# Kernel tuning notes

Measured on AMD Instinct MI355X. Metric: run time of the kernel, lower is better.

The kernel has to match this reference:

```python
import jax, jax.numpy as jnp
import numpy as np

D = 2048      # hidden_size
W = 4         # kernel_size
DG = 2048     # generator hidden size (no reduction)

def setup_inputs() -> dict:
    key = jax.random.key(0)
    k1, k2, k3, k4 = jax.random.split(key, 4)
    x = jax.random.normal(k1, (2, 4096, D), dtype=jnp.float32)
    # Linear weights stored torch-style [out, in]; scaled small for sane activations
    w1 = jax.random.normal(k2, (DG, D), dtype=jnp.float32) * 0.02
    w2 = jax.random.normal(k3, (D * W, DG), dtype=jnp.float32) * 0.02
    b2 = jax.random.normal(k4, (D * W,), dtype=jnp.float32) * 0.02
    return {"x": x, "w1": w1, "w2": w2, "b2": b2}

def reference(x, w1, w2, b2):
    B, T, Dh = x.shape
    # kernel generator: w2(silu(w1 @ x)) + b2 -> per-position kernels [B,T,D,W]
    h = jax.nn.silu(jnp.einsum('btd,gd->btg', x, w1))
    flat = jnp.einsum('btg,kg->btk', h, w2) + b2
    kernels = flat.reshape(B, T, Dh, W)
    # causal depthwise dynamic conv: y[b,t,d] = sum_w x[b, t-(W-1)+w, d] * k[b,t,d,w]
    xp = jnp.pad(x, ((0, 0), (W - 1, 0), (0, 0)))
    y = xp[:, 0:T, :] * kernels[..., 0]
    for w in range(1, W):  # small fixed-width loop over kernel taps
        y = y + xp[:, w:w + T, :] * kernels[..., w]
    return jax.nn.silu(y)
```

## Files before the change

### kernel.cpp

```cpp
#include <hip/hip_runtime.h>
#include <hip/hip_bf16.h>
#include <cstdint>

#define D_DIM  2048
#define T_DIM  4096
#define B_DIM  2
#define M_DIM  8192
#define DG_DIM 2048
#define N2_DIM 8192
#define K_DIM  2048

typedef __bf16 bf16x8 __attribute__((ext_vector_type(8)));
typedef __bf16 bf16x4 __attribute__((ext_vector_type(4)));
typedef float  f32x4  __attribute__((ext_vector_type(4)));

__device__ __forceinline__ void gload_lds16(const void* g, void* l) {
  __builtin_amdgcn_global_load_lds(
      (__attribute__((address_space(1))) void*)g,
      (__attribute__((address_space(3))) void*)l, 16, 0, 0);
}

__device__ __forceinline__ float silu_f(float a) {
  return a / (1.f + __expf(-a));
}

__global__ void cast_f32_bf16(const float* __restrict__ src,
                              __bf16* __restrict__ dst, int n4) {
  int i = blockIdx.x * blockDim.x + threadIdx.x;
  if (i >= n4) return;
  float4 v = ((const float4*)src)[i];
  bf16x4 o;
  o[0] = (__bf16)v.x; o[1] = (__bf16)v.y; o[2] = (__bf16)v.z; o[3] = (__bf16)v.w;
  ((bf16x4*)dst)[i] = o;
}

__global__ void cast_permute_w2(const float* __restrict__ src,
                                __bf16* __restrict__ dst, int n4) {
  int i = blockIdx.x * blockDim.x + threadIdx.x;
  if (i >= n4) return;
  const int row = i >> 9;
  const int pos = i & 511;
  const int blk = row >> 7, within = row & 127;
  const int wn = (within >> 6) & 1, j = (within >> 4) & 3, ln = within & 15;
  const int d = blk * 32 + wn * 16 + ln;
  const int k = 4 * d + j;
  float4 v = ((const float4*)src)[(size_t)k * 512 + pos];
  bf16x4 o;
  o[0] = (__bf16)v.x; o[1] = (__bf16)v.y; o[2] = (__bf16)v.z; o[3] = (__bf16)v.w;
  ((bf16x4*)dst)[i] = o;
}


__global__ __launch_bounds__(256) void gemm1_silu(
    const __bf16* __restrict__ A, const __bf16* __restrict__ B,
    __bf16* __restrict__ H) {
  constexpr int K = K_DIM, N = DG_DIM;
  __shared__ __bf16 sA[128 * 64];
  __shared__ __bf16 sB[128 * 64];
  const int tid  = threadIdx.x;
  const int lane = tid & 63;
  const int wv   = tid >> 6;
  const int wm   = wv >> 1, wn = wv & 1;
  const int ln   = lane & 15, qd = lane >> 4;
  const int m0 = blockIdx.y * 128, n0 = blockIdx.x * 128;

  f32x4 acc[4][4] = {};

  const int g  = lane >> 3;
  const int cl = lane & 7;
  const int cg = cl ^ g;
  const __bf16* gA[4];
  const __bf16* gB[4];
  int loff[4];
#pragma unroll
  for (int inst = 0; inst < 4; inst++) {
    const int r = (inst * 4 + wv) * 8 + g;
    gA[inst]   = A + (size_t)(m0 + r) * K + cg * 8;
    gB[inst]   = B + (size_t)(n0 + r) * K + cg * 8;
    loff[inst] = ((inst * 4 + wv) * 64 + lane) * 8;
  }

  for (int k0 = 0; k0 < K; k0 += 64) {
#pragma unroll
    for (int inst = 0; inst < 4; inst++)
      gload_lds16(gA[inst] + k0, sA + loff[inst]);
#pragma unroll
    for (int inst = 0; inst < 4; inst++)
      gload_lds16(gB[inst] + k0, sB + loff[inst]);
    __syncthreads();
#pragma unroll
    for (int h = 0; h < 2; h++) {
      bf16x8 af[4], bfr[4];
#pragma unroll
      for (int i = 0; i < 4; i++) {
        const int row = wm * 64 + i * 16 + ln;
        af[i] = *(const bf16x8*)(sA + row * 64 + (((h << 2) + qd) ^ (row & 7)) * 8);
      }
#pragma unroll
      for (int j = 0; j < 4; j++) {
        const int row = wn * 64 + j * 16 + ln;
        bfr[j] = *(const bf16x8*)(sB + row * 64 + (((h << 2) + qd) ^ (row & 7)) * 8);
      }
#pragma unroll
      for (int i = 0; i < 4; i++)
#pragma unroll
        for (int j = 0; j < 4; j++)
          acc[i][j] = __builtin_amdgcn_mfma_f32_16x16x32_bf16(af[i], bfr[j],
                                                              acc[i][j], 0, 0, 0);
    }
    __syncthreads();
  }

#pragma unroll
  for (int i = 0; i < 4; i++) {
#pragma unroll
    for (int j = 0; j < 4; j++) {
      const int col = n0 + wn * 64 + j * 16 + ln;
#pragma unroll
      for (int r = 0; r < 4; r++) {
        const int row = m0 + wm * 64 + i * 16 + qd * 4 + r;
        H[(size_t)row * N + col] = (__bf16)silu_f(acc[i][j][r]);
      }
    }
  }
}

__global__ __launch_bounds__(256) void gemm2_conv_silu(
    const __bf16* __restrict__ A, const __bf16* __restrict__ B,
    const float* __restrict__ b2, const float* __restrict__ x,
    float* __restrict__ out) {
  constexpr int K = K_DIM;
  __shared__ __bf16 sA[128 * 64];
  __shared__ __bf16 sB[128 * 64];
  const int tid  = threadIdx.x;
  const int lane = tid & 63;
  const int wv   = tid >> 6;
  const int wm   = wv >> 1, wn = wv & 1;
  const int ln   = lane & 15, qd = lane >> 4;
  const int m0 = blockIdx.y * 128, n0 = blockIdx.x * 128;

  f32x4 acc[4][4] = {};

  const int g  = lane >> 3;
  const int cl = lane & 7;
  const int cg = cl ^ g;
  const __bf16* gA[4];
  const __bf16* gB[4];
  int loff[4];
#pragma unroll
  for (int inst = 0; inst < 4; inst++) {
    const int r = (inst * 4 + wv) * 8 + g;
    gA[inst]   = A + (size_t)(m0 + r) * K + cg * 8;
    gB[inst]   = B + (size_t)(n0 + r) * K + cg * 8;
    loff[inst] = ((inst * 4 + wv) * 64 + lane) * 8;
  }

  for (int k0 = 0; k0 < K; k0 += 64) {
#pragma unroll
    for (int inst = 0; inst < 4; inst++)
      gload_lds16(gA[inst] + k0, sA + loff[inst]);
#pragma unroll
    for (int inst = 0; inst < 4; inst++)
      gload_lds16(gB[inst] + k0, sB + loff[inst]);
    __syncthreads();
#pragma unroll
    for (int h = 0; h < 2; h++) {
      bf16x8 af[4], bfr[4];
#pragma unroll
      for (int i = 0; i < 4; i++) {
        const int row = wm * 64 + i * 16 + ln;
        af[i] = *(const bf16x8*)(sA + row * 64 + (((h << 2) + qd) ^ (row & 7)) * 8);
      }
#pragma unroll
      for (int j = 0; j < 4; j++) {
        const int row = wn * 64 + j * 16 + ln;
        bfr[j] = *(const bf16x8*)(sB + row * 64 + (((h << 2) + qd) ^ (row & 7)) * 8);
      }
#pragma unroll
      for (int i = 0; i < 4; i++)
#pragma unroll
        for (int j = 0; j < 4; j++)
          acc[i][j] = __builtin_amdgcn_mfma_f32_16x16x32_bf16(af[i], bfr[j],
                                                              acc[i][j], 0, 0, 0);
    }
    __syncthreads();
  }

  const int d = (n0 >> 2) + wn * 16 + ln;
  const float4 bias = *(const float4*)(b2 + 4 * d);

#pragma unroll
  for (int i = 0; i < 4; i++) {
    const int m_base = m0 + wm * 64 + i * 16 + qd * 4;
    const int b  = m_base >> 12;
    const int tb = m_base & 4095;
    float xv[7];
#pragma unroll
    for (int s = 0; s < 7; s++) {
      const int tp = tb + s - 3;
      xv[s] = (tp >= 0) ? x[((size_t)((b << 12) + tp)) * D_DIM + d] : 0.f;
    }
#pragma unroll
    for (int r = 0; r < 4; r++) {
      float y = (acc[i][0][r] + bias.x) * xv[r + 0]
              + (acc[i][1][r] + bias.y) * xv[r + 1]
              + (acc[i][2][r] + bias.z) * xv[r + 2]
              + (acc[i][3][r] + bias.w) * xv[r + 3];
      out[(size_t)(m_base + r) * D_DIM + d] = silu_f(y);
    }
  }
}

extern "C" void kernel_launch(void* const* d_in, const int* in_sizes, int n_in,
                              void* d_out, int out_size, void* d_ws, size_t ws_size,
                              hipStream_t stream) {
  (void)in_sizes; (void)n_in; (void)out_size; (void)ws_size;
  const float* x  = (const float*)d_in[0];
  const float* w1 = (const float*)d_in[1];
  const float* w2 = (const float*)d_in[2];
  const float* b2 = (const float*)d_in[3];
  float* out = (float*)d_out;

  __bf16* xb  = (__bf16*)d_ws;
  __bf16* w1b = xb  + (size_t)M_DIM * D_DIM;
  __bf16* w2b = w1b + (size_t)DG_DIM * D_DIM;
  __bf16* hb  = w2b + (size_t)N2_DIM * DG_DIM;

  {
    int n4 = M_DIM * D_DIM / 4;
    cast_f32_bf16<<<(n4 + 255) / 256, 256, 0, stream>>>(x, xb, n4);
  }
  {
    int n4 = DG_DIM * D_DIM / 4;
    cast_f32_bf16<<<(n4 + 255) / 256, 256, 0, stream>>>(w1, w1b, n4);
  }
  {
    int n4 = N2_DIM * DG_DIM / 4;
    cast_permute_w2<<<(n4 + 255) / 256, 256, 0, stream>>>(w2, w2b, n4);
  }

  gemm1_silu<<<dim3(DG_DIM / 128, M_DIM / 128), 256, 0, stream>>>(xb, w1b, hb);
  gemm2_conv_silu<<<dim3(N2_DIM / 128, M_DIM / 128), 256, 0, stream>>>(
      hb, w2b, b2, x, out);
}
```

Baseline: 537.7 us.

## Switch GEMMs to 32x32x16 MFMA and fuse cast kernels into one launch

Both GEMM kernels move from 16x16x32 to 32x32x16 bf16 MFMA tiles with 2x2 accumulators per wave. This cuts LDS fragment loads per MFMA and the instruction count per k-step. The w2 permutation is reworked to fit the new accumulator layout, and the conv epilogue now combines tap pairs across lanes with a shuffle. The three cast kernels are merged into one launch to save launch overhead. In exchange, the epilogue issues more scattered single-element x loads, and only half the lanes write output.

```diff
diff --git a/kernel.cpp b/kernel.cpp
--- a/kernel.cpp
+++ b/kernel.cpp
@@ -12,7 +12,7 @@
 
 typedef __bf16 bf16x8 __attribute__((ext_vector_type(8)));
 typedef __bf16 bf16x4 __attribute__((ext_vector_type(4)));
-typedef float  f32x4  __attribute__((ext_vector_type(4)));
+typedef float  f32x16 __attribute__((ext_vector_type(16)));
 
 __device__ __forceinline__ void gload_lds16(const void* g, void* l) {
   __builtin_amdgcn_global_load_lds(
@@ -24,30 +24,40 @@
   return a / (1.f + __expf(-a));
 }
 
-__global__ void cast_f32_bf16(const float* __restrict__ src,
-                              __bf16* __restrict__ dst, int n4) {
+#define NX4  (M_DIM * D_DIM / 4)
+#define NW14 (DG_DIM * D_DIM / 4)
+#define NW24 (N2_DIM * DG_DIM / 4)
+
+__global__ void cast_all(const float* __restrict__ x, const float* __restrict__ w1,
+                         const float* __restrict__ w2, __bf16* __restrict__ xb,
+                         __bf16* __restrict__ w1b, __bf16* __restrict__ w2b) {
   int i = blockIdx.x * blockDim.x + threadIdx.x;
-  if (i >= n4) return;
-  float4 v = ((const float4*)src)[i];
+  const float4* src;
+  bf16x4* dst;
+  if (i < NX4) {
+    src = (const float4*)x + i;
+    dst = (bf16x4*)xb + i;
+  } else if (i < NX4 + NW14) {
+    int i2 = i - NX4;
+    src = (const float4*)w1 + i2;
+    dst = (bf16x4*)w1b + i2;
+  } else {
+    int i3 = i - (NX4 + NW14);
+    if (i3 >= NW24) return;
+    const int row = i3 >> 9;
+    const int pos = i3 & 511;
+    const int Bk = row >> 7;
+    const int wn = (row >> 6) & 1, jn = (row >> 5) & 1;
+    const int cl4 = (row >> 4) & 1, dl = row & 15;
+    const int d = 32 * Bk + 16 * wn + dl;
+    const int k = 4 * d + cl4 + 2 * jn;
+    src = (const float4*)w2 + (size_t)k * 512 + pos;
+    dst = (bf16x4*)w2b + i3;
+  }
+  float4 v = *src;
   bf16x4 o;
   o[0] = (__bf16)v.x; o[1] = (__bf16)v.y; o[2] = (__bf16)v.z; o[3] = (__bf16)v.w;
-  ((bf16x4*)dst)[i] = o;
-}
-
-__global__ void cast_permute_w2(const float* __restrict__ src,
-                                __bf16* __restrict__ dst, int n4) {
-  int i = blockIdx.x * blockDim.x + threadIdx.x;
-  if (i >= n4) return;
-  const int row = i >> 9;
-  const int pos = i & 511;
-  const int blk = row >> 7, within = row & 127;
-  const int wn = (within >> 6) & 1, j = (within >> 4) & 3, ln = within & 15;
-  const int d = blk * 32 + wn * 16 + ln;
-  const int k = 4 * d + j;
-  float4 v = ((const float4*)src)[(size_t)k * 512 + pos];
-  bf16x4 o;
-  o[0] = (__bf16)v.x; o[1] = (__bf16)v.y; o[2] = (__bf16)v.z; o[3] = (__bf16)v.w;
-  ((bf16x4*)dst)[i] = o;
+  *dst = o;
 }
 
 
@@ -61,10 +71,10 @@
   const int lane = tid & 63;
   const int wv   = tid >> 6;
   const int wm   = wv >> 1, wn = wv & 1;
-  const int ln   = lane & 15, qd = lane >> 4;
+  const int cl31 = lane & 31, kh = lane >> 5;
   const int m0 = blockIdx.y * 128, n0 = blockIdx.x * 128;
 
-  f32x4 acc[4][4] = {};
+  f32x16 acc[2][2] = {};
 
   const int g  = lane >> 3;
   const int cl = lane & 7;
@@ -89,37 +99,38 @@
       gload_lds16(gB[inst] + k0, sB + loff[inst]);
     __syncthreads();
 #pragma unroll
-    for (int h = 0; h < 2; h++) {
-      bf16x8 af[4], bfr[4];
-#pragma unroll
-      for (int i = 0; i < 4; i++) {
-        const int row = wm * 64 + i * 16 + ln;
-        af[i] = *(const bf16x8*)(sA + row * 64 + (((h << 2) + qd) ^ (row & 7)) * 8);
-      }
-#pragma unroll
-      for (int j = 0; j < 4; j++) {
-        const int row = wn * 64 + j * 16 + ln;
-        bfr[j] = *(const bf16x8*)(sB + row * 64 + (((h << 2) + qd) ^ (row & 7)) * 8);
-      }
-#pragma unroll
-      for (int i = 0; i < 4; i++)
-#pragma unroll
-        for (int j = 0; j < 4; j++)
-          acc[i][j] = __builtin_amdgcn_mfma_f32_16x16x32_bf16(af[i], bfr[j],
-                                                              acc[i][j], 0, 0, 0);
-    }
-    __syncthreads();
-  }
-
-#pragma unroll
-  for (int i = 0; i < 4; i++) {
-#pragma unroll
-    for (int j = 0; j < 4; j++) {
-      const int col = n0 + wn * 64 + j * 16 + ln;
-#pragma unroll
-      for (int r = 0; r < 4; r++) {
-        const int row = m0 + wm * 64 + i * 16 + qd * 4 + r;
-        H[(size_t)row * N + col] = (__bf16)silu_f(acc[i][j][r]);
+    for (int ks = 0; ks < 4; ks++) {
+      const int chunk = ks * 2 + kh;
+      bf16x8 af[2], bq[2];
+#pragma unroll
+      for (int im = 0; im < 2; im++) {
+        const int row = wm * 64 + im * 32 + cl31;
+        af[im] = *(const bf16x8*)(sA + row * 64 + ((chunk ^ (row & 7)) * 8));
+      }
+#pragma unroll
+      for (int jn = 0; jn < 2; jn++) {
+        const int row = wn * 64 + jn * 32 + cl31;
+        bq[jn] = *(const bf16x8*)(sB + row * 64 + ((chunk ^ (row & 7)) * 8));
+      }
+#pragma unroll
+      for (int im = 0; im < 2; im++)
+#pragma unroll
+        for (int jn = 0; jn < 2; jn++)
+          acc[im][jn] = __builtin_amdgcn_mfma_f32_32x32x16_bf16(
+              af[im], bq[jn], acc[im][jn], 0, 0, 0);
+    }
+    __syncthreads();
+  }
+
+#pragma unroll
+  for (int im = 0; im < 2; im++) {
+#pragma unroll
+    for (int jn = 0; jn < 2; jn++) {
+      const int col = n0 + wn * 64 + jn * 32 + cl31;
+#pragma unroll
+      for (int reg = 0; reg < 16; reg++) {
+        const int row = m0 + wm * 64 + im * 32 + 4 * kh + (reg & 3) + 8 * (reg >> 2);
+        H[(size_t)row * N + col] = (__bf16)silu_f(acc[im][jn][reg]);
       }
     }
   }
@@ -136,10 +147,10 @@
   const int lane = tid & 63;
   const int wv   = tid >> 6;
   const int wm   = wv >> 1, wn = wv & 1;
-  const int ln   = lane & 15, qd = lane >> 4;
+  const int cl31 = lane & 31, kh = lane >> 5;
   const int m0 = blockIdx.y * 128, n0 = blockIdx.x * 128;
 
-  f32x4 acc[4][4] = {};
+  f32x16 acc[2][2] = {};
 
   const int g  = lane >> 3;
   const int cl = lane & 7;
@@ -164,49 +175,53 @@
       gload_lds16(gB[inst] + k0, sB + loff[inst]);
     __syncthreads();
 #pragma unroll
-    for (int h = 0; h < 2; h++) {
-      bf16x8 af[4], bfr[4];
-#pragma unroll
-      for (int i = 0; i < 4; i++) {
-        const int row = wm * 64 + i * 16 + ln;
-        af[i] = *(const bf16x8*)(sA + row * 64 + (((h << 2) + qd) ^ (row & 7)) * 8);
-      }
-#pragma unroll
-      for (int j = 0; j < 4; j++) {
-        const int row = wn * 64 + j * 16 + ln;
-        bfr[j] = *(const bf16x8*)(sB + row * 64 + (((h << 2) + qd) ^ (row & 7)) * 8);
-      }
-#pragma unroll
-      for (int i = 0; i < 4; i++)
-#pragma unroll
-        for (int j = 0; j < 4; j++)
-          acc[i][j] = __builtin_amdgcn_mfma_f32_16x16x32_bf16(af[i], bfr[j],
-                                                              acc[i][j], 0, 0, 0);
-    }
-    __syncthreads();
-  }
-
-  const int d = (n0 >> 2) + wn * 16 + ln;
-  const float4 bias = *(const float4*)(b2 + 4 * d);
-
-#pragma unroll
-  for (int i = 0; i < 4; i++) {
-    const int m_base = m0 + wm * 64 + i * 16 + qd * 4;
-    const int b  = m_base >> 12;
-    const int tb = m_base & 4095;
-    float xv[7];
-#pragma unroll
-    for (int s = 0; s < 7; s++) {
-      const int tp = tb + s - 3;
-      xv[s] = (tp >= 0) ? x[((size_t)((b << 12) + tp)) * D_DIM + d] : 0.f;
-    }
-#pragma unroll
-    for (int r = 0; r < 4; r++) {
-      float y = (acc[i][0][r] + bias.x) * xv[r + 0]
-              + (acc[i][1][r] + bias.y) * xv[r + 1]
-              + (acc[i][2][r] + bias.z) * xv[r + 2]
-              + (acc[i][3][r] + bias.w) * xv[r + 3];
-      out[(size_t)(m_base + r) * D_DIM + d] = silu_f(y);
+    for (int ks = 0; ks < 4; ks++) {
+      const int chunk = ks * 2 + kh;
+      bf16x8 af[2], bq[2];
+#pragma unroll
+      for (int im = 0; im < 2; im++) {
+        const int row = wm * 64 + im * 32 + cl31;
+        af[im] = *(const bf16x8*)(sA + row * 64 + ((chunk ^ (row & 7)) * 8));
+      }
+#pragma unroll
+      for (int jn = 0; jn < 2; jn++) {
+        const int row = wn * 64 + jn * 32 + cl31;
+        bq[jn] = *(const bf16x8*)(sB + row * 64 + ((chunk ^ (row & 7)) * 8));
+      }
+#pragma unroll
+      for (int im = 0; im < 2; im++)
+#pragma unroll
+        for (int jn = 0; jn < 2; jn++)
+          acc[im][jn] = __builtin_amdgcn_mfma_f32_32x32x16_bf16(
+              af[im], bq[jn], acc[im][jn], 0, 0, 0);
+    }
+    __syncthreads();
+  }
+
+  const int dl  = lane & 15;
+  const int cl4 = (lane >> 4) & 1;
+  const int d   = (n0 >> 2) + wn * 16 + dl;
+  const float b_lo = b2[4 * d + cl4];
+  const float b_hi = b2[4 * d + cl4 + 2];
+
+#pragma unroll
+  for (int im = 0; im < 2; im++) {
+    const int m_blk = m0 + wm * 64 + im * 32 + 4 * kh;
+    const int b  = m_blk >> 12;
+    const int tb = m_blk & 4095;
+    const float* xb_ = x + ((size_t)b << 12) * D_DIM + d;
+    float* ob_ = out + ((size_t)m_blk) * D_DIM + d;
+#pragma unroll
+    for (int reg = 0; reg < 16; reg++) {
+      const int ro = (reg & 3) + 8 * (reg >> 2);
+      const int tr = tb + ro;
+      const int t0 = tr + cl4 - 3;
+      const int t1 = tr + cl4 - 1;
+      const float xv0 = (t0 >= 0) ? xb_[(size_t)t0 * D_DIM] : 0.f;
+      const float xv1 = (t1 >= 0) ? xb_[(size_t)t1 * D_DIM] : 0.f;
+      float p = (acc[im][0][reg] + b_lo) * xv0 + (acc[im][1][reg] + b_hi) * xv1;
+      p += __shfl_xor(p, 16);
+      if (cl4 == 0) ob_[(size_t)ro * D_DIM] = silu_f(p);
     }
   }
 }
@@ -227,16 +242,8 @@
   __bf16* hb  = w2b + (size_t)N2_DIM * DG_DIM;
 
   {
-    int n4 = M_DIM * D_DIM / 4;
-    cast_f32_bf16<<<(n4 + 255) / 256, 256, 0, stream>>>(x, xb, n4);
-  }
-  {
-    int n4 = DG_DIM * D_DIM / 4;
-    cast_f32_bf16<<<(n4 + 255) / 256, 256, 0, stream>>>(w1, w1b, n4);
-  }
-  {
-    int n4 = N2_DIM * DG_DIM / 4;
-    cast_permute_w2<<<(n4 + 255) / 256, 256, 0, stream>>>(w2, w2b, n4);
+    int total = NX4 + NW14 + NW24;
+    cast_all<<<(total + 255) / 256, 256, 0, stream>>>(x, w1, w2, xb, w1b, w2b);
   }
 
   gemm1_silu<<<dim3(DG_DIM / 128, M_DIM / 128), 256, 0, stream>>>(xb, w1b, hb);
```

New measurement: 624.1 us. 1.16x slower.
